# Optimization experiments

Hardware: AMD Instinct MI355X
Metric: run time of the kernel (lower is better)

The kernel has to match this reference:

```python
import jax, jax.numpy as jnp
import numpy as np

B, SRC, TGT = 1024, 50, 25
I, H = 69, 1024          # input_size = 54 dofs + 15 actions; rnn_size
T = SRC + TGT - 1        # 74 frames total


def gru_cell(x, h, w_ih, w_hh, b_ih, b_hh):
    # PyTorch GRUCell math
    gi = x @ w_ih.T + b_ih            # [B, 3H]
    gh = h @ w_hh.T + b_hh            # [B, 3H]
    i_r, i_z, i_n = jnp.split(gi, 3, axis=-1)
    h_r, h_z, h_n = jnp.split(gh, 3, axis=-1)
    r = jax.nn.sigmoid(i_r + h_r)
    z = jax.nn.sigmoid(i_z + h_z)
    n = jnp.tanh(i_n + r * h_n)
    return (1.0 - z) * n + z * h


def setup_inputs() -> dict:
    key = jax.random.key(0)
    ks = jax.random.split(key, 10)
    s_ih = 1.0 / np.sqrt(H)
    return {
        "encoder_inputs": jax.random.normal(ks[0], (B, SRC, I), jnp.float32),
        "decoder_output": jax.random.normal(ks[1], (B, TGT - 1, I), jnp.float32),
        "w_ih": jax.random.uniform(ks[2], (3 * H, I), jnp.float32, -s_ih, s_ih),
        "w_hh": jax.random.uniform(ks[3], (3 * H, H), jnp.float32, -s_ih, s_ih),
        "b_ih": jax.random.uniform(ks[4], (3 * H,), jnp.float32, -s_ih, s_ih),
        "b_hh": jax.random.uniform(ks[5], (3 * H,), jnp.float32, -s_ih, s_ih),
        "fc1_w": jax.random.uniform(ks[6], (I, H), jnp.float32, -s_ih, s_ih),
        "fc1_b": jax.random.uniform(ks[7], (I,), jnp.float32, -s_ih, s_ih),
        "fc2_w": jax.random.uniform(ks[8], (1, I * T), jnp.float32, -0.01, 0.01),
        "fc2_b": jax.random.uniform(ks[9], (1,), jnp.float32, -0.01, 0.01),
    }


def reference(encoder_inputs, decoder_output, w_ih, w_hh, b_ih, b_hh,
              fc1_w, fc1_b, fc2_w, fc2_b):
    # Dropout is identity in eval mode; faithful deterministic reference.
    all_frame = jnp.concatenate([encoder_inputs, decoder_output], axis=1)  # [B,T,I]
    frames = jnp.transpose(all_frame, (1, 0, 2))                           # [T,B,I]
    batch = encoder_inputs.shape[0]
    state0 = jnp.zeros((batch, H), jnp.float32)

    # Encoding pass: GRU over all T frames
    def step1(h, x):
        return gru_cell(x, h, w_ih, w_hh, b_ih, b_hh), None
    state, _ = jax.lax.scan(step1, state0, frames)

    inp0 = frames[0]
    state = gru_cell(inp0, state, w_ih, w_hh, b_ih, b_hh)
    out0 = inp0 + state @ fc1_w.T + fc1_b

    def step2(carry, _):
        h, prev = carry
        h2 = gru_cell(prev, h, w_ih, w_hh, b_ih, b_hh)
        out = prev + h2 @ fc1_w.T + fc1_b
        return (h2, out), out
    _, rest = jax.lax.scan(step2, (state, out0), None, length=T - 1)

    outputs = jnp.concatenate([out0[None], rest], axis=0)   # [T,B,I]
    base = jnp.transpose(outputs, (1, 0, 2)).reshape(batch, -1)  # [B, T*I]
    logit = base @ fc2_w.T + fc2_b                           # [B,1]
    return jax.nn.sigmoid(logit)
```

## Files before the change

### kernel.cpp

```cpp
#include <hip/hip_runtime.h>
#include <hip/hip_bf16.h>

#define Bsz  1024
#define Hsz  1024
#define Isz  69
#define Tn   74
#define KP   1152
#define XP   128
#define XPF  80
#define XLP  84

typedef short  short8 __attribute__((ext_vector_type(8)));
typedef float  f32x4  __attribute__((ext_vector_type(4)));
using ushort = unsigned short;

__device__ __forceinline__ ushort f2bf(float f) {
    unsigned u = __float_as_uint(f);
    return (ushort)((u + 0x7fffu + ((u >> 16) & 1u)) >> 16);
}
__device__ __forceinline__ float bf2f(ushort u) {
    return __uint_as_float((unsigned)u << 16);
}

__device__ __forceinline__ void gld_lds16(const void* g, void* l) {
    __builtin_amdgcn_global_load_lds(
        (const __attribute__((address_space(1))) unsigned int*)g,
        (__attribute__((address_space(3))) unsigned int*)l, 16, 0, 0);
}

__global__ void init_k(ushort* __restrict__ hbf, float* __restrict__ logit,
                       const float* __restrict__ fc2_b) {
    unsigned gid = blockIdx.x * 256 + threadIdx.x;
    if (gid < 1024u * 1024u) hbf[gid] = 0;
    if (gid < 1024u) logit[gid] = fc2_b[0];
}

__global__ void pack_w(const float* __restrict__ w_ih, const float* __restrict__ w_hh,
                       const float* __restrict__ fc1_w,
                       ushort* __restrict__ wpack, ushort* __restrict__ w1p) {
    unsigned gid = blockIdx.x * 256 + threadIdx.x;
    const unsigned WN4 = 3072u * 288u;
    if (gid < WN4) {
        unsigned row = gid / 288u, c4 = (gid % 288u) * 4u;
        ushort4 o; ushort* po = (ushort*)&o;
#pragma unroll
        for (int e = 0; e < 4; ++e) {
            unsigned k = c4 + e; float v = 0.f;
            if (k < 1024u)       v = w_hh[(size_t)row * 1024u + k];
            else if (k < 1093u)  v = w_ih[(size_t)row * 69u + (k - 1024u)];
            po[e] = f2bf(v);
        }
        *(ushort4*)(wpack + (size_t)row * KP + c4) = o;
    } else if (gid < WN4 + 20480u) {
        unsigned g2 = gid - WN4;
        unsigned i = g2 / 256u, c4 = (g2 % 256u) * 4u;
        ushort4 o; ushort* po = (ushort*)&o;
#pragma unroll
        for (int e = 0; e < 4; ++e)
            po[e] = (i < 69u) ? f2bf(fc1_w[(size_t)i * 1024u + c4 + e]) : (ushort)0;
        *(ushort4*)(w1p + (size_t)i * 1024u + c4) = o;
    }
}

__global__ void pack_f(const float* __restrict__ enc, const float* __restrict__ dec,
                       ushort* __restrict__ frames, float* __restrict__ x0f) {
    unsigned gid = blockIdx.x * 256 + threadIdx.x;
    const unsigned NF4 = 74u * 1024u * 32u;
    if (gid < NF4) {
        unsigned c4 = (gid & 31u) * 4u;
        unsigned b  = (gid >> 5) & 1023u;
        unsigned tf = gid >> 15;
        ushort4 o; ushort* po = (ushort*)&o;
#pragma unroll
        for (int e = 0; e < 4; ++e) {
            unsigned i = c4 + e; float v = 0.f;
            if (i < 69u)
                v = (tf < 50u) ? enc[((size_t)b * 50u + tf) * 69u + i]
                               : dec[((size_t)b * 24u + (tf - 50u)) * 69u + i];
            po[e] = f2bf(v);
        }
        *(ushort4*)(frames + (size_t)tf * 1024u * XP + (size_t)b * XP + c4) = o;
    } else if (gid < NF4 + 81920u) {
        unsigned g2 = gid - NF4;
        unsigned b = g2 / 80u, i = g2 % 80u;
        x0f[g2] = (i < 69u) ? enc[(size_t)b * 50u * 69u + i] : 0.f;
    }
}

__launch_bounds__(512, 2)
__global__ void gru_fused(
    const ushort* __restrict__ hbf,
    const ushort* __restrict__ xframe, const float* __restrict__ xprevG,
    const ushort* __restrict__ wpack, const ushort* __restrict__ w1p,
    const float* __restrict__ b_ih, const float* __restrict__ b_hh,
    const float* __restrict__ fc1_b, const float* __restrict__ fc2_w,
    ushort* __restrict__ hbf_out,
    float* __restrict__ xoutG, float* __restrict__ logitG, int d)
{
    __shared__ __align__(16) ushort ldsH[8 * 8192];
    __shared__ __align__(16) float  xLf[64 * XLP];

    const int t    = threadIdx.x;
    const int blk  = blockIdx.x;
    const int idx  = blk >> 3, xcd = blk & 7;
    const int bn   = xcd * 2 + (idx & 1);
    const int bm   = idx >> 1;
    const int wave = t >> 6, lane = t & 63;
    const int wk   = wave >> 2, wn = wave & 3;
    const int quad = lane >> 4, l16 = lane & 15;
    const int p_   = lane & 15, rl_ = lane >> 4;

#pragma unroll
    for (int c = 0; c < 8; ++c) {
#pragma unroll
        for (int i2 = 0; i2 < 2; ++i2) {
            const int srow = wave * 8 + i2 * 4 + rl_;
            const int cc   = p_ ^ (srow & 15);
            const ushort* g = hbf + (size_t)(bm * 64 + srow) * 1024 + c * 128 + cc * 8;
            gld_lds16(g, &ldsH[c * 8192 + (wave * 8 + i2 * 4) * 128]);
        }
    }

    const ushort* bp0 = wpack + (size_t)(bn * 64 + wn * 16 + l16) * KP + quad * 8 + wk * 64;
    const ushort* bp1 = bp0 + (size_t)1024 * KP;
    const ushort* bp2 = bp0 + (size_t)2048 * KP;
    short8 bq[2][3];
    bq[0][0] = *(const short8*)(bp0);      bq[0][1] = *(const short8*)(bp1);      bq[0][2] = *(const short8*)(bp2);
    bq[1][0] = *(const short8*)(bp0 + 32); bq[1][1] = *(const short8*)(bp1 + 32); bq[1][2] = *(const short8*)(bp2 + 32);

    short8 xf_[4][2];
    float  xp[4][4];
    if (d < 1) {
#pragma unroll
        for (int kk = 0; kk < 2; ++kk) {
            const int gg = (wk * 2 + kk) * 4 + quad;
#pragma unroll
            for (int mt = 0; mt < 4; ++mt)
                xf_[mt][kk] = *(const short8*)(xframe + (size_t)(bm * 64 + mt * 16 + l16) * XP + gg * 8);
        }
    } else if (wave < 5) {
        const int j = wave * 16 + l16;
#pragma unroll
        for (int fm = 0; fm < 4; ++fm)
#pragma unroll
            for (int r = 0; r < 4; ++r)
                xp[fm][r] = xprevG[(size_t)(bm * 64 + fm * 16 + quad * 4 + r) * XPF + j];
    }
    __syncthreads();

    f32x4 accR[4], accZ[4], accNH[4], accNI[4];
#pragma unroll
    for (int i = 0; i < 4; ++i) {
        accR[i]  = (f32x4){0.f,0.f,0.f,0.f}; accZ[i]  = (f32x4){0.f,0.f,0.f,0.f};
        accNH[i] = (f32x4){0.f,0.f,0.f,0.f}; accNI[i] = (f32x4){0.f,0.f,0.f,0.f};
    }

#define MFMA_BF16 __builtin_amdgcn_mfma_f32_16x16x32_bf16
#pragma unroll
    for (int c = 0; c < 8; ++c) {
#pragma unroll
        for (int kk = 0; kk < 2; ++kk) {
            const int g   = (wk * 2 + kk) * 4 + quad;
            const ushort* ab = &ldsH[c * 8192];
            const int pos = (g ^ l16) * 8;
            short8 a0 = *(const short8*)(ab + ( 0 + l16) * 128 + pos);
            short8 a1 = *(const short8*)(ab + (16 + l16) * 128 + pos);
            short8 a2 = *(const short8*)(ab + (32 + l16) * 128 + pos);
            short8 a3 = *(const short8*)(ab + (48 + l16) * 128 + pos);
            short8 b0 = bq[kk][0], b1v = bq[kk][1], b2v = bq[kk][2];
            bq[kk][0] = *(const short8*)(bp0 + (c + 1) * 128 + kk * 32);
            bq[kk][1] = *(const short8*)(bp1 + (c + 1) * 128 + kk * 32);
            bq[kk][2] = *(const short8*)(bp2 + (c + 1) * 128 + kk * 32);
            accR[0] = MFMA_BF16(a0, b0, accR[0],0,0,0);
            accZ[0] = MFMA_BF16(a0, b1v, accZ[0],0,0,0);
            accNH[0]= MFMA_BF16(a0, b2v, accNH[0],0,0,0);
            accR[1] = MFMA_BF16(a1, b0, accR[1],0,0,0);
            accZ[1] = MFMA_BF16(a1, b1v, accZ[1],0,0,0);
            accNH[1]= MFMA_BF16(a1, b2v, accNH[1],0,0,0);
            accR[2] = MFMA_BF16(a2, b0, accR[2],0,0,0);
            accZ[2] = MFMA_BF16(a2, b1v, accZ[2],0,0,0);
            accNH[2]= MFMA_BF16(a2, b2v, accNH[2],0,0,0);
            accR[3] = MFMA_BF16(a3, b0, accR[3],0,0,0);
            accZ[3] = MFMA_BF16(a3, b1v, accZ[3],0,0,0);
            accNH[3]= MFMA_BF16(a3, b2v, accNH[3],0,0,0);
        }
    }

    if (d >= 1 && wave < 5) {
        const int j = wave * 16 + l16;
        const ushort* bfp = w1p + (size_t)j * 1024 + quad * 8;
        f32x4 facc[4];
#pragma unroll
        for (int i = 0; i < 4; ++i) facc[i] = (f32x4){0.f,0.f,0.f,0.f};
#pragma unroll
        for (int c = 0; c < 8; ++c) {
#pragma unroll
            for (int q4 = 0; q4 < 4; ++q4) {
                short8 bb = *(const short8*)(bfp + c * 128 + q4 * 32);
#pragma unroll
                for (int fm = 0; fm < 4; ++fm) {
                    const int row = fm * 16 + l16;
                    short8 aa = *(const short8*)(&ldsH[c * 8192 + row * 128 + (((q4 * 4 + quad) ^ l16) * 8)]);
                    facc[fm] = MFMA_BF16(aa, bb, facc[fm],0,0,0);
                }
            }
        }
        const float b1f = (j < Isz) ? fc1_b[j] : 0.f;
#pragma unroll
        for (int fm = 0; fm < 4; ++fm)
#pragma unroll
            for (int r = 0; r < 4; ++r) {
                const int m = fm * 16 + quad * 4 + r;
                xLf[m * XLP + j] = (j < Isz) ? (xp[fm][r] + facc[fm][r] + b1f) : 0.f;
            }
    }
    __syncthreads();

    if (d >= 1 && bn == 0) {
        for (int i = t; i < 64 * XPF; i += 512) {
            const int r = i / XPF, c2 = i % XPF;
            xoutG[(size_t)(bm * 64 + r) * XPF + c2] = xLf[r * XLP + c2];
        }
    }

    if (d >= 1) {
#pragma unroll
        for (int kk = 0; kk < 2; ++kk) {
            const int gg = (wk * 2 + kk) * 4 + quad;
#pragma unroll
            for (int mt = 0; mt < 4; ++mt) {
                short8 a = (short8){0,0,0,0,0,0,0,0};
                if (gg < 10) {
                    const float* p = &xLf[(mt * 16 + l16) * XLP + gg * 8];
                    f32x4 v0 = *(const f32x4*)p;
                    f32x4 v1 = *(const f32x4*)(p + 4);
                    union { short8 s; ushort u[8]; } uu;
                    uu.u[0] = f2bf(v0[0]); uu.u[1] = f2bf(v0[1]);
                    uu.u[2] = f2bf(v0[2]); uu.u[3] = f2bf(v0[3]);
                    uu.u[4] = f2bf(v1[0]); uu.u[5] = f2bf(v1[1]);
                    uu.u[6] = f2bf(v1[2]); uu.u[7] = f2bf(v1[3]);
                    a = uu.s;
                }
                xf_[mt][kk] = a;
            }
        }
    }
#pragma unroll
    for (int kk = 0; kk < 2; ++kk) {
        short8 b0 = bq[kk][0], b1v = bq[kk][1], b2v = bq[kk][2];
        accR[0] = MFMA_BF16(xf_[0][kk], b0, accR[0],0,0,0);
        accZ[0] = MFMA_BF16(xf_[0][kk], b1v, accZ[0],0,0,0);
        accNI[0]= MFMA_BF16(xf_[0][kk], b2v, accNI[0],0,0,0);
        accR[1] = MFMA_BF16(xf_[1][kk], b0, accR[1],0,0,0);
        accZ[1] = MFMA_BF16(xf_[1][kk], b1v, accZ[1],0,0,0);
        accNI[1]= MFMA_BF16(xf_[1][kk], b2v, accNI[1],0,0,0);
        accR[2] = MFMA_BF16(xf_[2][kk], b0, accR[2],0,0,0);
        accZ[2] = MFMA_BF16(xf_[2][kk], b1v, accZ[2],0,0,0);
        accNI[2]= MFMA_BF16(xf_[2][kk], b2v, accNI[2],0,0,0);
        accR[3] = MFMA_BF16(xf_[3][kk], b0, accR[3],0,0,0);
        accZ[3] = MFMA_BF16(xf_[3][kk], b1v, accZ[3],0,0,0);
        accNI[3]= MFMA_BF16(xf_[3][kk], b2v, accNI[3],0,0,0);
    }

    f32x4* exch = (f32x4*)ldsH;
    const int slot = wn * 64 + lane;
    {
        const int mtb = wk ? 0 : 2;
        f32x4* w = exch + wk * 2048;
#pragma unroll
        for (int i = 0; i < 2; ++i) {
            const int mt = mtb + i;
            w[(i * 4 + 0) * 256 + slot] = accR[mt];
            w[(i * 4 + 1) * 256 + slot] = accZ[mt];
            w[(i * 4 + 2) * 256 + slot] = accNH[mt];
            w[(i * 4 + 3) * 256 + slot] = accNI[mt];
        }
    }
    const int jcol = bn * 64 + wn * 16 + l16;
    const int mto  = wk * 2;
    float hp[2][4];
#pragma unroll
    for (int i = 0; i < 2; ++i)
#pragma unroll
        for (int r = 0; r < 4; ++r)
            hp[i][r] = bf2f(hbf[(size_t)(bm * 64 + (mto + i) * 16 + quad * 4 + r) * 1024 + jcol]);
    __syncthreads();

    {
        const f32x4* rd = exch + (wk ^ 1) * 2048;
        const float bir = b_ih[jcol],        bhr = b_hh[jcol];
        const float biz = b_ih[1024 + jcol], bhz = b_hh[1024 + jcol];
        const float bin_= b_ih[2048 + jcol], bhn = b_hh[2048 + jcol];
#pragma unroll
        for (int i = 0; i < 2; ++i) {
            const int mt = mto + i;
            f32x4 aR = accR[mt] + rd[(i * 4 + 0) * 256 + slot];
            f32x4 aZ = accZ[mt] + rd[(i * 4 + 1) * 256 + slot];
            f32x4 aH = accNH[mt]+ rd[(i * 4 + 2) * 256 + slot];
            f32x4 aI = accNI[mt]+ rd[(i * 4 + 3) * 256 + slot];
#pragma unroll
            for (int r = 0; r < 4; ++r) {
                const int m = bm * 64 + mt * 16 + quad * 4 + r;
                float gr = aR[r] + bir + bhr;
                float gz = aZ[r] + biz + bhz;
                float rg = 1.f / (1.f + __expf(-gr));
                float zg = 1.f / (1.f + __expf(-gz));
                float nx = aI[r] + bin_ + rg * (aH[r] + bhn);
                nx = fminf(30.f, fmaxf(-30.f, nx));
                float e  = __expf(-2.f * nx);
                float ng = (1.f - e) / (1.f + e);
                float hn = (1.f - zg) * ng + zg * hp[i][r];
                hbf_out[(size_t)m * 1024 + jcol] = f2bf(hn);
            }
        }
    }

    if (d >= 1 && bn == 0 && wave == 5) {
        const int row = lane;
        float lp = 0.f;
        for (int c2 = 0; c2 < Isz; ++c2)
            lp += fc2_w[(size_t)(d - 1) * Isz + c2] * xLf[row * XLP + c2];
        logitG[bm * 64 + row] += lp;
    }
#undef MFMA_BF16
}

__launch_bounds__(512)
__global__ void tail_k(const ushort* __restrict__ hbf, const float* __restrict__ xprevG,
                       const ushort* __restrict__ w1p, const float* __restrict__ fc1_b,
                       const float* __restrict__ fc2_w, const float* __restrict__ logitG,
                       float* __restrict__ outp)
{
    __shared__ __align__(16) ushort ldsH[8 * 8192];
    __shared__ __align__(16) float  xLf[64 * XLP];
    const int t    = threadIdx.x;
    const int bm   = blockIdx.x;
    const int wave = t >> 6, lane = t & 63;
    const int quad = lane >> 4, l16 = lane & 15;
    const int p_   = lane & 15, rl_ = lane >> 4;

#pragma unroll
    for (int c = 0; c < 8; ++c) {
#pragma unroll
        for (int i2 = 0; i2 < 2; ++i2) {
            const int srow = wave * 8 + i2 * 4 + rl_;
            const int cc   = p_ ^ (srow & 15);
            const ushort* g = hbf + (size_t)(bm * 64 + srow) * 1024 + c * 128 + cc * 8;
            gld_lds16(g, &ldsH[c * 8192 + (wave * 8 + i2 * 4) * 128]);
        }
    }
    float xp[4][4];
    if (wave < 5) {
        const int j = wave * 16 + l16;
#pragma unroll
        for (int fm = 0; fm < 4; ++fm)
#pragma unroll
            for (int r = 0; r < 4; ++r)
                xp[fm][r] = xprevG[(size_t)(bm * 64 + fm * 16 + quad * 4 + r) * XPF + j];
    }
    __syncthreads();
    if (wave < 5) {
        const int j = wave * 16 + l16;
        const ushort* bfp = w1p + (size_t)j * 1024 + quad * 8;
        f32x4 facc[4];
#pragma unroll
        for (int i = 0; i < 4; ++i) facc[i] = (f32x4){0.f,0.f,0.f,0.f};
#pragma unroll
        for (int c = 0; c < 8; ++c) {
#pragma unroll
            for (int q4 = 0; q4 < 4; ++q4) {
                short8 bb = *(const short8*)(bfp + c * 128 + q4 * 32);
#pragma unroll
                for (int fm = 0; fm < 4; ++fm) {
                    const int row = fm * 16 + l16;
                    short8 aa = *(const short8*)(&ldsH[c * 8192 + row * 128 + (((q4 * 4 + quad) ^ l16) * 8)]);
                    facc[fm] = __builtin_amdgcn_mfma_f32_16x16x32_bf16(aa, bb, facc[fm],0,0,0);
                }
            }
        }
        const float b1f = (j < Isz) ? fc1_b[j] : 0.f;
#pragma unroll
        for (int fm = 0; fm < 4; ++fm)
#pragma unroll
            for (int r = 0; r < 4; ++r) {
                const int m = fm * 16 + quad * 4 + r;
                xLf[m * XLP + j] = (j < Isz) ? (xp[fm][r] + facc[fm][r] + b1f) : 0.f;
            }
    }
    __syncthreads();
    if (t < 64) {
        float lp = 0.f;
        for (int c2 = 0; c2 < Isz; ++c2)
            lp += fc2_w[(size_t)73 * Isz + c2] * xLf[t * XLP + c2];
        outp[bm * 64 + t] = 1.f / (1.f + __expf(-(logitG[bm * 64 + t] + lp)));
    }
}

extern "C" void kernel_launch(void* const* d_in, const int* in_sizes, int n_in,
                              void* d_out, int out_size, void* d_ws, size_t ws_size,
                              hipStream_t stream)
{
    const float* enc   = (const float*)d_in[0];
    const float* dec   = (const float*)d_in[1];
    const float* w_ih  = (const float*)d_in[2];
    const float* w_hh  = (const float*)d_in[3];
    const float* b_ih  = (const float*)d_in[4];
    const float* b_hh  = (const float*)d_in[5];
    const float* fc1_w = (const float*)d_in[6];
    const float* fc1_b = (const float*)d_in[7];
    const float* fc2_w = (const float*)d_in[8];
    const float* fc2_b = (const float*)d_in[9];
    float* out = (float*)d_out;

    char* ws = (char*)d_ws;
    size_t off = 0;
    auto alloc = [&](size_t bytes) -> void* {
        void* p = ws + off; off += (bytes + 255) & ~(size_t)255; return p;
    };
    ushort* wpack  = (ushort*)alloc((size_t)3072 * KP * 2);
    ushort* w1p    = (ushort*)alloc((size_t)80 * 1024 * 2);
    ushort* frames = (ushort*)alloc((size_t)Tn * 1024 * XP * 2);
    float*  x0f    = (float*) alloc((size_t)1024 * XPF * 4);
    ushort* hbfA   = (ushort*)alloc((size_t)1024 * 1024 * 2);
    ushort* hbfB   = (ushort*)alloc((size_t)1024 * 1024 * 2);
    float*  xGA    = (float*) alloc((size_t)1024 * XPF * 4);
    float*  xGB    = (float*) alloc((size_t)1024 * XPF * 4);
    float*  logit  = (float*) alloc((size_t)1024 * 4);

    init_k<<<4096, 256, 0, stream>>>(hbfA, logit, fc2_b);
    pack_w<<<3536, 256, 0, stream>>>(w_ih, w_hh, fc1_w, wpack, w1p);
    pack_f<<<9792, 256, 0, stream>>>(enc, dec, frames, x0f);

    ushort* hb_c = hbfA; ushort* hb_n = hbfB;

    for (int tt = 0; tt < Tn + 1; ++tt) {
        const ushort* xfr = frames + (size_t)(tt < Tn ? tt : 0) * 1024 * XP;
        gru_fused<<<256, 512, 0, stream>>>(hb_c, xfr, x0f, wpack, w1p,
                                           b_ih, b_hh, fc1_b, fc2_w,
                                           hb_n, xGA, logit, 0);
        { ushort* tb = hb_c; hb_c = hb_n; hb_n = tb; }
    }
    for (int d = 1; d < Tn; ++d) {
        const float* xin  = (d == 1) ? x0f : ((d & 1) ? xGB : xGA);
        float*       xout = (d & 1) ? xGA : xGB;
        gru_fused<<<256, 512, 0, stream>>>(hb_c, frames, xin, wpack, w1p,
                                           b_ih, b_hh, fc1_b, fc2_w,
                                           hb_n, xout, logit, d);
        { ushort* tb = hb_c; hb_c = hb_n; hb_n = tb; }
    }
    tail_k<<<16, 512, 0, stream>>>(hb_c, xGA, w1p, fc1_b, fc2_w, logit, out);
}
```

Before: 4.121 ms.

## Halve batch tile per block and drop split-K LDS reduction in GRU step

Each block now handles 32 batch rows with 4 waves (256 threads) instead of 64 rows with 8 waves, doubling the grid to 512 blocks. Each wave now covers the full K range for its 16 output columns, so the cross-wave LDS exchange of partial accumulators and its extra barrier go away. The fc1 projection is spread over all four waves, with wave 0 taking a fifth tile. The cost is that every weight tile is read by twice as many blocks, and each wave runs a longer serial K loop.

```diff
diff --git a/kernel.cpp b/kernel.cpp
--- a/kernel.cpp
+++ b/kernel.cpp
@@ -87,7 +87,7 @@
     }
 }
 
-__launch_bounds__(512, 2)
+__launch_bounds__(256, 2)
 __global__ void gru_fused(
     const ushort* __restrict__ hbf,
     const ushort* __restrict__ xframe, const float* __restrict__ xprevG,
@@ -97,8 +97,8 @@
     ushort* __restrict__ hbf_out,
     float* __restrict__ xoutG, float* __restrict__ logitG, int d)
 {
-    __shared__ __align__(16) ushort ldsH[8 * 8192];
-    __shared__ __align__(16) float  xLf[64 * XLP];
+    __shared__ __align__(16) ushort ldsH[8 * 4096];
+    __shared__ __align__(16) float  xLf[32 * XLP];
 
     const int t    = threadIdx.x;
     const int blk  = blockIdx.x;
@@ -106,7 +106,6 @@
     const int bn   = xcd * 2 + (idx & 1);
     const int bm   = idx >> 1;
     const int wave = t >> 6, lane = t & 63;
-    const int wk   = wave >> 2, wn = wave & 3;
     const int quad = lane >> 4, l16 = lane & 15;
     const int p_   = lane & 15, rl_ = lane >> 4;
 
@@ -116,119 +115,121 @@
         for (int i2 = 0; i2 < 2; ++i2) {
             const int srow = wave * 8 + i2 * 4 + rl_;
             const int cc   = p_ ^ (srow & 15);
-            const ushort* g = hbf + (size_t)(bm * 64 + srow) * 1024 + c * 128 + cc * 8;
-            gld_lds16(g, &ldsH[c * 8192 + (wave * 8 + i2 * 4) * 128]);
-        }
-    }
-
-    const ushort* bp0 = wpack + (size_t)(bn * 64 + wn * 16 + l16) * KP + quad * 8 + wk * 64;
+            const ushort* g = hbf + (size_t)(bm * 32 + srow) * 1024 + c * 128 + cc * 8;
+            gld_lds16(g, &ldsH[c * 4096 + (wave * 8 + i2 * 4) * 128]);
+        }
+    }
+
+    const ushort* bp0 = wpack + (size_t)(bn * 64 + wave * 16 + l16) * KP + quad * 8;
     const ushort* bp1 = bp0 + (size_t)1024 * KP;
     const ushort* bp2 = bp0 + (size_t)2048 * KP;
     short8 bq[2][3];
     bq[0][0] = *(const short8*)(bp0);      bq[0][1] = *(const short8*)(bp1);      bq[0][2] = *(const short8*)(bp2);
     bq[1][0] = *(const short8*)(bp0 + 32); bq[1][1] = *(const short8*)(bp1 + 32); bq[1][2] = *(const short8*)(bp2 + 32);
 
-    short8 xf_[4][2];
-    float  xp[4][4];
+    short8 xf_[2][4];
+    float  xp0[2][4], xp1[2][4];
     if (d < 1) {
 #pragma unroll
-        for (int kk = 0; kk < 2; ++kk) {
-            const int gg = (wk * 2 + kk) * 4 + quad;
-#pragma unroll
-            for (int mt = 0; mt < 4; ++mt)
-                xf_[mt][kk] = *(const short8*)(xframe + (size_t)(bm * 64 + mt * 16 + l16) * XP + gg * 8);
-        }
-    } else if (wave < 5) {
+        for (int kk = 0; kk < 4; ++kk) {
+            const int gg = kk * 4 + quad;
+#pragma unroll
+            for (int mt = 0; mt < 2; ++mt)
+                xf_[mt][kk] = *(const short8*)(xframe + (size_t)(bm * 32 + mt * 16 + l16) * XP + gg * 8);
+        }
+    } else {
         const int j = wave * 16 + l16;
 #pragma unroll
-        for (int fm = 0; fm < 4; ++fm)
+        for (int fm = 0; fm < 2; ++fm)
 #pragma unroll
             for (int r = 0; r < 4; ++r)
-                xp[fm][r] = xprevG[(size_t)(bm * 64 + fm * 16 + quad * 4 + r) * XPF + j];
+                xp0[fm][r] = xprevG[(size_t)(bm * 32 + fm * 16 + quad * 4 + r) * XPF + j];
+        if (wave == 0) {
+            const int j4 = 64 + l16;
+#pragma unroll
+            for (int fm = 0; fm < 2; ++fm)
+#pragma unroll
+                for (int r = 0; r < 4; ++r)
+                    xp1[fm][r] = xprevG[(size_t)(bm * 32 + fm * 16 + quad * 4 + r) * XPF + j4];
+        }
     }
     __syncthreads();
 
-    f32x4 accR[4], accZ[4], accNH[4], accNI[4];
-#pragma unroll
-    for (int i = 0; i < 4; ++i) {
+    f32x4 accR[2], accZ[2], accNH[2], accNI[2];
+#pragma unroll
+    for (int i = 0; i < 2; ++i) {
         accR[i]  = (f32x4){0.f,0.f,0.f,0.f}; accZ[i]  = (f32x4){0.f,0.f,0.f,0.f};
         accNH[i] = (f32x4){0.f,0.f,0.f,0.f}; accNI[i] = (f32x4){0.f,0.f,0.f,0.f};
     }
 
 #define MFMA_BF16 __builtin_amdgcn_mfma_f32_16x16x32_bf16
 #pragma unroll
-    for (int c = 0; c < 8; ++c) {
-#pragma unroll
-        for (int kk = 0; kk < 2; ++kk) {
-            const int g   = (wk * 2 + kk) * 4 + quad;
-            const ushort* ab = &ldsH[c * 8192];
-            const int pos = (g ^ l16) * 8;
-            short8 a0 = *(const short8*)(ab + ( 0 + l16) * 128 + pos);
-            short8 a1 = *(const short8*)(ab + (16 + l16) * 128 + pos);
-            short8 a2 = *(const short8*)(ab + (32 + l16) * 128 + pos);
-            short8 a3 = *(const short8*)(ab + (48 + l16) * 128 + pos);
-            short8 b0 = bq[kk][0], b1v = bq[kk][1], b2v = bq[kk][2];
-            bq[kk][0] = *(const short8*)(bp0 + (c + 1) * 128 + kk * 32);
-            bq[kk][1] = *(const short8*)(bp1 + (c + 1) * 128 + kk * 32);
-            bq[kk][2] = *(const short8*)(bp2 + (c + 1) * 128 + kk * 32);
-            accR[0] = MFMA_BF16(a0, b0, accR[0],0,0,0);
-            accZ[0] = MFMA_BF16(a0, b1v, accZ[0],0,0,0);
-            accNH[0]= MFMA_BF16(a0, b2v, accNH[0],0,0,0);
-            accR[1] = MFMA_BF16(a1, b0, accR[1],0,0,0);
-            accZ[1] = MFMA_BF16(a1, b1v, accZ[1],0,0,0);
-            accNH[1]= MFMA_BF16(a1, b2v, accNH[1],0,0,0);
-            accR[2] = MFMA_BF16(a2, b0, accR[2],0,0,0);
-            accZ[2] = MFMA_BF16(a2, b1v, accZ[2],0,0,0);
-            accNH[2]= MFMA_BF16(a2, b2v, accNH[2],0,0,0);
-            accR[3] = MFMA_BF16(a3, b0, accR[3],0,0,0);
-            accZ[3] = MFMA_BF16(a3, b1v, accZ[3],0,0,0);
-            accNH[3]= MFMA_BF16(a3, b2v, accNH[3],0,0,0);
-        }
-    }
-
-    if (d >= 1 && wave < 5) {
-        const int j = wave * 16 + l16;
-        const ushort* bfp = w1p + (size_t)j * 1024 + quad * 8;
-        f32x4 facc[4];
-#pragma unroll
-        for (int i = 0; i < 4; ++i) facc[i] = (f32x4){0.f,0.f,0.f,0.f};
-#pragma unroll
-        for (int c = 0; c < 8; ++c) {
-#pragma unroll
-            for (int q4 = 0; q4 < 4; ++q4) {
-                short8 bb = *(const short8*)(bfp + c * 128 + q4 * 32);
-#pragma unroll
-                for (int fm = 0; fm < 4; ++fm) {
-                    const int row = fm * 16 + l16;
-                    short8 aa = *(const short8*)(&ldsH[c * 8192 + row * 128 + (((q4 * 4 + quad) ^ l16) * 8)]);
-                    facc[fm] = MFMA_BF16(aa, bb, facc[fm],0,0,0);
+    for (int q = 0; q < 32; ++q) {
+        const int c  = q >> 2;
+        const ushort* ab = &ldsH[c * 4096];
+        const int g2 = (q & 3) * 4 + quad;
+        const int pos = (g2 ^ l16) * 8;
+        short8 a0 = *(const short8*)(ab + ( 0 + l16) * 128 + pos);
+        short8 a1 = *(const short8*)(ab + (16 + l16) * 128 + pos);
+        short8 b0 = bq[q & 1][0], b1v = bq[q & 1][1], b2v = bq[q & 1][2];
+        {
+            bq[q & 1][0] = *(const short8*)(bp0 + (q + 2) * 32);
+            bq[q & 1][1] = *(const short8*)(bp1 + (q + 2) * 32);
+            bq[q & 1][2] = *(const short8*)(bp2 + (q + 2) * 32);
+        }
+        accR[0] = MFMA_BF16(a0, b0, accR[0],0,0,0);
+        accZ[0] = MFMA_BF16(a0, b1v, accZ[0],0,0,0);
+        accNH[0]= MFMA_BF16(a0, b2v, accNH[0],0,0,0);
+        accR[1] = MFMA_BF16(a1, b0, accR[1],0,0,0);
+        accZ[1] = MFMA_BF16(a1, b1v, accZ[1],0,0,0);
+        accNH[1]= MFMA_BF16(a1, b2v, accNH[1],0,0,0);
+    }
+
+    if (d >= 1) {
+        auto fc1_tile = [&](int j, float (*xpv)[4]) {
+            const ushort* bfp = w1p + (size_t)j * 1024 + quad * 8;
+            f32x4 facc[2];
+            facc[0] = (f32x4){0.f,0.f,0.f,0.f}; facc[1] = (f32x4){0.f,0.f,0.f,0.f};
+#pragma unroll
+            for (int c = 0; c < 8; ++c) {
+#pragma unroll
+                for (int q4 = 0; q4 < 4; ++q4) {
+                    short8 bb = *(const short8*)(bfp + c * 128 + q4 * 32);
+#pragma unroll
+                    for (int fm = 0; fm < 2; ++fm) {
+                        const int row = fm * 16 + l16;
+                        short8 aa = *(const short8*)(&ldsH[c * 4096 + row * 128 + (((q4 * 4 + quad) ^ l16) * 8)]);
+                        facc[fm] = MFMA_BF16(aa, bb, facc[fm],0,0,0);
+                    }
                 }
             }
-        }
-        const float b1f = (j < Isz) ? fc1_b[j] : 0.f;
-#pragma unroll
-        for (int fm = 0; fm < 4; ++fm)
-#pragma unroll
-            for (int r = 0; r < 4; ++r) {
-                const int m = fm * 16 + quad * 4 + r;
-                xLf[m * XLP + j] = (j < Isz) ? (xp[fm][r] + facc[fm][r] + b1f) : 0.f;
-            }
+            const float b1f = (j < Isz) ? fc1_b[j] : 0.f;
+#pragma unroll
+            for (int fm = 0; fm < 2; ++fm)
+#pragma unroll
+                for (int r = 0; r < 4; ++r) {
+                    const int m = fm * 16 + quad * 4 + r;
+                    xLf[m * XLP + j] = (j < Isz) ? (xpv[fm][r] + facc[fm][r] + b1f) : 0.f;
+                }
+        };
+        fc1_tile(wave * 16 + l16, xp0);
+        if (wave == 0) fc1_tile(64 + l16, xp1);
     }
     __syncthreads();
 
     if (d >= 1 && bn == 0) {
-        for (int i = t; i < 64 * XPF; i += 512) {
+        for (int i = t; i < 32 * XPF; i += 256) {
             const int r = i / XPF, c2 = i % XPF;
-            xoutG[(size_t)(bm * 64 + r) * XPF + c2] = xLf[r * XLP + c2];
+            xoutG[(size_t)(bm * 32 + r) * XPF + c2] = xLf[r * XLP + c2];
         }
     }
 
     if (d >= 1) {
 #pragma unroll
-        for (int kk = 0; kk < 2; ++kk) {
-            const int gg = (wk * 2 + kk) * 4 + quad;
-#pragma unroll
-            for (int mt = 0; mt < 4; ++mt) {
+        for (int kk = 0; kk < 4; ++kk) {
+            const int gg = kk * 4 + quad;
+#pragma unroll
+            for (int mt = 0; mt < 2; ++mt) {
                 short8 a = (short8){0,0,0,0,0,0,0,0};
                 if (gg < 10) {
                     const float* p = &xLf[(mt * 16 + l16) * XLP + gg * 8];
@@ -246,81 +247,56 @@
         }
     }
 #pragma unroll
-    for (int kk = 0; kk < 2; ++kk) {
-        short8 b0 = bq[kk][0], b1v = bq[kk][1], b2v = bq[kk][2];
+    for (int kk = 0; kk < 4; ++kk) {
+        short8 b0 = bq[kk & 1][0], b1v = bq[kk & 1][1], b2v = bq[kk & 1][2];
+        if (kk < 2) {
+            bq[kk & 1][0] = *(const short8*)(bp0 + (34 + kk) * 32);
+            bq[kk & 1][1] = *(const short8*)(bp1 + (34 + kk) * 32);
+            bq[kk & 1][2] = *(const short8*)(bp2 + (34 + kk) * 32);
+        }
         accR[0] = MFMA_BF16(xf_[0][kk], b0, accR[0],0,0,0);
         accZ[0] = MFMA_BF16(xf_[0][kk], b1v, accZ[0],0,0,0);
         accNI[0]= MFMA_BF16(xf_[0][kk], b2v, accNI[0],0,0,0);
         accR[1] = MFMA_BF16(xf_[1][kk], b0, accR[1],0,0,0);
         accZ[1] = MFMA_BF16(xf_[1][kk], b1v, accZ[1],0,0,0);
         accNI[1]= MFMA_BF16(xf_[1][kk], b2v, accNI[1],0,0,0);
-        accR[2] = MFMA_BF16(xf_[2][kk], b0, accR[2],0,0,0);
-        accZ[2] = MFMA_BF16(xf_[2][kk], b1v, accZ[2],0,0,0);
-        accNI[2]= MFMA_BF16(xf_[2][kk], b2v, accNI[2],0,0,0);
-        accR[3] = MFMA_BF16(xf_[3][kk], b0, accR[3],0,0,0);
-        accZ[3] = MFMA_BF16(xf_[3][kk], b1v, accZ[3],0,0,0);
-        accNI[3]= MFMA_BF16(xf_[3][kk], b2v, accNI[3],0,0,0);
-    }
-
-    f32x4* exch = (f32x4*)ldsH;
-    const int slot = wn * 64 + lane;
+    }
+
+    if (d >= 1 && bn == 0 && wave == 3 && lane < 32) {
+        float lp = 0.f;
+        for (int c2 = 0; c2 < Isz; ++c2)
+            lp += fc2_w[(size_t)(d - 1) * Isz + c2] * xLf[lane * XLP + c2];
+        logitG[bm * 32 + lane] += lp;
+    }
+
     {
-        const int mtb = wk ? 0 : 2;
-        f32x4* w = exch + wk * 2048;
-#pragma unroll
-        for (int i = 0; i < 2; ++i) {
-            const int mt = mtb + i;
-            w[(i * 4 + 0) * 256 + slot] = accR[mt];
-            w[(i * 4 + 1) * 256 + slot] = accZ[mt];
-            w[(i * 4 + 2) * 256 + slot] = accNH[mt];
-            w[(i * 4 + 3) * 256 + slot] = accNI[mt];
-        }
-    }
-    const int jcol = bn * 64 + wn * 16 + l16;
-    const int mto  = wk * 2;
-    float hp[2][4];
-#pragma unroll
-    for (int i = 0; i < 2; ++i)
-#pragma unroll
-        for (int r = 0; r < 4; ++r)
-            hp[i][r] = bf2f(hbf[(size_t)(bm * 64 + (mto + i) * 16 + quad * 4 + r) * 1024 + jcol]);
-    __syncthreads();
-
-    {
-        const f32x4* rd = exch + (wk ^ 1) * 2048;
+        const int jcol = bn * 64 + wave * 16 + l16;
         const float bir = b_ih[jcol],        bhr = b_hh[jcol];
         const float biz = b_ih[1024 + jcol], bhz = b_hh[1024 + jcol];
         const float bin_= b_ih[2048 + jcol], bhn = b_hh[2048 + jcol];
-#pragma unroll
-        for (int i = 0; i < 2; ++i) {
-            const int mt = mto + i;
-            f32x4 aR = accR[mt] + rd[(i * 4 + 0) * 256 + slot];
-            f32x4 aZ = accZ[mt] + rd[(i * 4 + 1) * 256 + slot];
-            f32x4 aH = accNH[mt]+ rd[(i * 4 + 2) * 256 + slot];
-            f32x4 aI = accNI[mt]+ rd[(i * 4 + 3) * 256 + slot];
+        float hp[2][4];
+#pragma unroll
+        for (int mt = 0; mt < 2; ++mt)
+#pragma unroll
+            for (int r = 0; r < 4; ++r)
+                hp[mt][r] = bf2f(hbf[(size_t)(bm * 32 + mt * 16 + quad * 4 + r) * 1024 + jcol]);
+#pragma unroll
+        for (int mt = 0; mt < 2; ++mt) {
 #pragma unroll
             for (int r = 0; r < 4; ++r) {
-                const int m = bm * 64 + mt * 16 + quad * 4 + r;
-                float gr = aR[r] + bir + bhr;
-                float gz = aZ[r] + biz + bhz;
+                const int m = bm * 32 + mt * 16 + quad * 4 + r;
+                float gr = accR[mt][r] + bir + bhr;
+                float gz = accZ[mt][r] + biz + bhz;
                 float rg = 1.f / (1.f + __expf(-gr));
                 float zg = 1.f / (1.f + __expf(-gz));
-                float nx = aI[r] + bin_ + rg * (aH[r] + bhn);
+                float nx = accNI[mt][r] + bin_ + rg * (accNH[mt][r] + bhn);
                 nx = fminf(30.f, fmaxf(-30.f, nx));
                 float e  = __expf(-2.f * nx);
                 float ng = (1.f - e) / (1.f + e);
-                float hn = (1.f - zg) * ng + zg * hp[i][r];
+                float hn = (1.f - zg) * ng + zg * hp[mt][r];
                 hbf_out[(size_t)m * 1024 + jcol] = f2bf(hn);
             }
         }
-    }
-
-    if (d >= 1 && bn == 0 && wave == 5) {
-        const int row = lane;
-        float lp = 0.f;
-        for (int c2 = 0; c2 < Isz; ++c2)
-            lp += fc2_w[(size_t)(d - 1) * Isz + c2] * xLf[row * XLP + c2];
-        logitG[bm * 64 + row] += lp;
     }
 #undef MFMA_BF16
 }
@@ -435,7 +411,7 @@
 
     for (int tt = 0; tt < Tn + 1; ++tt) {
         const ushort* xfr = frames + (size_t)(tt < Tn ? tt : 0) * 1024 * XP;
-        gru_fused<<<256, 512, 0, stream>>>(hb_c, xfr, x0f, wpack, w1p,
+        gru_fused<<<512, 256, 0, stream>>>(hb_c, xfr, x0f, wpack, w1p,
                                            b_ih, b_hh, fc1_b, fc2_w,
                                            hb_n, xGA, logit, 0);
         { ushort* tb = hb_c; hb_c = hb_n; hb_n = tb; }
@@ -443,7 +419,7 @@
     for (int d = 1; d < Tn; ++d) {
         const float* xin  = (d == 1) ? x0f : ((d & 1) ? xGB : xGA);
         float*       xout = (d & 1) ? xGA : xGB;
-        gru_fused<<<256, 512, 0, stream>>>(hb_c, frames, xin, wpack, w1p,
+        gru_fused<<<512, 256, 0, stream>>>(hb_c, frames, xin, wpack, w1p,
                                            b_ih, b_hh, fc1_b, fc2_w,
                                            hb_n, xout, logit, d);
         { ushort* tb = hb_c; hb_c = hb_n; hb_n = tb; }
```

After: 7.135 ms. 73.1% more time.
